# Performance work log

Measured on AMD Instinct MI355X. Metric: run time of the kernel, lower is better.

Reference implementation:

```python
import jax, jax.numpy as jnp
import numpy as np

N = 65536      # total atoms
D = 1024       # hidden_size (encoder output dim)
H = 2048       # ffn_hidden_size
OUT = 1        # output_size
M = 4096       # number of molecules (segments)


def _lin(k, fi, fo):
    return jax.random.normal(k, (fi, fo), jnp.float32) * (1.0 / np.sqrt(fi))


def setup_inputs() -> dict:
    key = jax.random.key(0)
    ks = jax.random.split(key, 14)
    hidden = jax.random.normal(ks[0], (N, D), jnp.float32)
    segment_ids = jnp.sort(jax.random.randint(ks[1], (N,), 0, M)).astype(jnp.int64)
    inp = {
        "hidden": hidden,
        "ffn_W1": _lin(ks[2], D, H), "ffn_b1": jnp.zeros((H,), jnp.float32),
        "ffn_W2": _lin(ks[3], H, H), "ffn_b2": jnp.zeros((H,), jnp.float32),
        "ffn_W3": _lin(ks[4], H, OUT), "ffn_b3": jnp.zeros((OUT,), jnp.float32),
        "wr_W1": _lin(ks[5], D, H), "wr_b1": jnp.zeros((H,), jnp.float32),
        "wr_W2": _lin(ks[6], H, H), "wr_b2": jnp.zeros((H,), jnp.float32),
        "wr_W3": _lin(ks[7], H, OUT), "wr_b3": jnp.ones((OUT,), jnp.float32),  # bias=1 keeps segment weight sums away from 0
        "segment_ids": segment_ids,
    }
    return inp


def _ffn(x, W1, b1, W2, b2, W3, b3):
    # Dropout(p) is identity in eval; activation = ReLU
    h = jax.nn.relu(x @ W1 + b1)
    h = jax.nn.relu(h @ W2 + b2)
    return h @ W3 + b3


def reference(hidden, ffn_W1, ffn_b1, ffn_W2, ffn_b2, ffn_W3, ffn_b3,
              wr_W1, wr_b1, wr_W2, wr_b2, wr_W3, wr_b3, segment_ids):
    seg = segment_ids.astype(jnp.int32)
    output = _ffn(hidden, ffn_W1, ffn_b1, ffn_W2, ffn_b2, ffn_W3, ffn_b3)   # [N, OUT]
    weights = _ffn(hidden, wr_W1, wr_b1, wr_W2, wr_b2, wr_W3, wr_b3)        # [N, OUT]
    # per-molecule sums over ALL elements of the segment slice (matches .sum())
    out_sum = jax.ops.segment_sum(output.sum(-1), seg, num_segments=M)      # [M]
    w_sum = jax.ops.segment_sum(weights.sum(-1), seg, num_segments=M)       # [M]
    ratio = (out_sum / w_sum)[seg][:, None]                                 # [N, 1]
    return output - weights * ratio
```

## Files before the change

kernel.cpp:

```cpp
#include <hip/hip_runtime.h>
#include <hip/hip_bf16.h>

#define DEVINL __device__ __forceinline__

typedef __attribute__((ext_vector_type(8))) short s8v;
typedef __attribute__((ext_vector_type(4))) float f4v;

using bf16 = __hip_bfloat16;
typedef unsigned short u16;

DEVINL u16 f2bu(float f) {
  bf16 h = __float2bfloat16(f);
  return *reinterpret_cast<u16*>(&h);
}

DEVINL void gload16(const void* g, void* l) {
  __builtin_amdgcn_global_load_lds((const __attribute__((address_space(1))) void*)g,
                                   (__attribute__((address_space(3))) void*)l, 16, 0, 0);
}

#define BAR()    __builtin_amdgcn_s_barrier()
#define LGKM0()  asm volatile("s_waitcnt lgkmcnt(0)" ::: "memory")
#define VM(n)    asm volatile("s_waitcnt vmcnt(" #n ")" ::: "memory")
#define SCHED0() __builtin_amdgcn_sched_barrier(0)

__global__ void k_f32_to_bf16(const float* __restrict__ x, u16* __restrict__ y, long n4) {
  long i = (long)blockIdx.x * blockDim.x + threadIdx.x;
  if (i >= n4) return;
  float4 v = ((const float4*)x)[i];
  ushort4 o;
  o.x = f2bu(v.x); o.y = f2bu(v.y); o.z = f2bu(v.z); o.w = f2bu(v.w);
  ((ushort4*)y)[i] = o;
}

__global__ void k_transpose_bf16(const float* __restrict__ W, u16* __restrict__ Wt,
                                 int rows, int cols) {
  __shared__ float tile[32][33];
  const int tx = threadIdx.x, ty = threadIdx.y;
  const int c0 = blockIdx.x * 32, r0 = blockIdx.y * 32;
  #pragma unroll
  for (int i = ty; i < 32; i += 8)
    tile[i][tx] = W[(long)(r0 + i) * cols + (c0 + tx)];
  __syncthreads();
  #pragma unroll
  for (int i = ty; i < 32; i += 8)
    Wt[(long)(c0 + i) * rows + (r0 + tx)] = f2bu(tile[tx][i]);
}

extern __shared__ char smem[];

template<int EPI>
__global__ __launch_bounds__(512, 2)
void k_gemm8(const u16* __restrict__ A, const u16* __restrict__ Bt,
             u16* __restrict__ C, const float* __restrict__ bias,
             const float* __restrict__ w3, float* __restrict__ oacc,
             int N, int K) {
  const int tid = threadIdx.x;
  const int w = tid >> 6, lane = tid & 63;
  const int id = blockIdx.x;
  const int cpx = gridDim.x >> 3;
  const int sw = (id & 7) * cpx + (id >> 3);
  const int bn = sw & 7, bm = sw >> 3;

  const int wm = (w >> 2) * 128, wn = (w & 3) * 64;
  const int nt = K >> 6;

  f4v acc[8][4];
  #pragma unroll
  for (int i = 0; i < 8; ++i)
    #pragma unroll
    for (int jj = 0; jj < 4; ++jj)
      #pragma unroll
      for (int r = 0; r < 4; ++r) acc[i][jj][r] = 0.f;

  const int rowl = tid >> 2;
  const int jsw = (tid & 3) ^ ((rowl >> 1) & 3);
  const u16* gA = A + (long)(bm * 256 + rowl) * K + jsw * 8;
  const u16* gB = Bt + (long)(bn * 256 + rowl) * K + jsw * 8;
  const long cstr = (long)128 * K;
  const uint wb = (uint)w * 1024u;

  const uint swz = ((uint)((lane >> 4) ^ ((lane >> 1) & 3))) * 16u;
  const uint aoff = (uint)(wm + (lane & 15)) * 64u + swz;
  const uint boff = (uint)(wn + (lane & 15)) * 64u + swz + 32768u;

#define STAGE_A(pp, ks, t) do { \
    const u16* g_ = gA + (long)(t) * 64 + (ks) * 32; \
    char* l_ = smem + (uint)(pp) * 65536u + (uint)(ks) * 16384u + wb; \
    gload16(g_, l_); gload16(g_ + cstr, l_ + 8192); } while (0)
#define STAGE_B(pp, ks, t) do { \
    const u16* g_ = gB + (long)(t) * 64 + (ks) * 32; \
    char* l_ = smem + (uint)(pp) * 65536u + 32768u + (uint)(ks) * 16384u + wb; \
    gload16(g_, l_); gload16(g_ + cstr, l_ + 8192); } while (0)

#define RD_A(dst, base, ksb) do { \
    _Pragma("unroll") \
    for (int mi_ = 0; mi_ < 8; ++mi_) \
      dst[mi_] = *(const s8v*)(smem + (base) + (ksb) + aoff + (uint)mi_ * 1024u); } while (0)
#define RD_B(dst, base, ksb, c0) do { \
    dst[0] = *(const s8v*)(smem + (base) + (ksb) + boff + (uint)(c0) * 1024u); \
    dst[1] = *(const s8v*)(smem + (base) + (ksb) + boff + (uint)((c0) + 1) * 1024u); } while (0)

#define MFMA8(A_, B_, c0i, c1i) do { \
    __builtin_amdgcn_s_setprio(1); \
    _Pragma("unroll") \
    for (int mi_ = 0; mi_ < 8; ++mi_) { \
      acc[mi_][c0i] = __builtin_amdgcn_mfma_f32_16x16x32_bf16(A_[mi_], B_[0], acc[mi_][c0i], 0, 0, 0); \
      acc[mi_][c1i] = __builtin_amdgcn_mfma_f32_16x16x32_bf16(A_[mi_], B_[1], acc[mi_][c1i], 0, 0, 0); \
    } \
    __builtin_amdgcn_s_setprio(0); } while (0)

  s8v a[8], b01[2], b23[2];

  STAGE_A(0, 0, 0); STAGE_B(0, 0, 0); STAGE_A(0, 1, 0); STAGE_B(0, 1, 0);
  if (nt > 1) { STAGE_A(1, 0, 1); STAGE_B(1, 0, 1); VM(8); }
  else        { VM(4); }
  BAR();

  for (int t = 0; t < nt; ++t) {
    const int p = t & 1, q = p ^ 1;
    const uint pb = (uint)p * 65536u;
    RD_A(a, pb, 0u); RD_B(b01, pb, 0u, 0);
    if (t + 1 < nt) STAGE_A(q, 1, t + 1);
    BAR(); LGKM0(); SCHED0();
    MFMA8(a, b01, 0, 1);
    BAR();
    RD_B(b23, pb, 0u, 2);
    if (t + 1 < nt) { STAGE_B(q, 1, t + 1); VM(8); }
    else            { VM(0); }
    BAR(); LGKM0(); SCHED0();
    MFMA8(a, b23, 2, 3);
    BAR();
    RD_A(a, pb, 16384u); RD_B(b01, pb, 16384u, 0);
    if (t + 2 < nt) STAGE_A(p, 0, t + 2);
    BAR(); LGKM0(); SCHED0();
    MFMA8(a, b01, 0, 1);
    BAR();
    RD_B(b23, pb, 16384u, 2);
    if (t + 2 < nt)      { STAGE_B(p, 0, t + 2); VM(8); }
    else if (t + 1 < nt) { VM(4); }
    else                 { VM(0); }
    BAR(); LGKM0(); SCHED0();
    MFMA8(a, b23, 2, 3);
    BAR();
  }

  const int crow = bm * 256 + wm + ((lane >> 4) << 2);
  const int ccol = bn * 256 + wn + (lane & 15);
  if (EPI == 1) {
    #pragma unroll
    for (int jj = 0; jj < 4; ++jj) {
      const float bb = bias[ccol + jj * 16];
      #pragma unroll
      for (int mi = 0; mi < 8; ++mi)
        #pragma unroll
        for (int r = 0; r < 4; ++r) {
          float v = acc[mi][jj][r] + bb;
          v = v > 0.f ? v : 0.f;
          C[(long)(crow + mi * 16 + r) * N + ccol + jj * 16] = f2bu(v);
        }
    }
  } else {
    float bb[4], ww[4];
    #pragma unroll
    for (int jj = 0; jj < 4; ++jj) { bb[jj] = bias[ccol + jj * 16]; ww[jj] = w3[ccol + jj * 16]; }
    #pragma unroll
    for (int mi = 0; mi < 8; ++mi)
      #pragma unroll
      for (int r = 0; r < 4; ++r) {
        float s = 0.f;
        #pragma unroll
        for (int jj = 0; jj < 4; ++jj) {
          float v = acc[mi][jj][r] + bb[jj];
          v = v > 0.f ? v : 0.f;
          s += v * ww[jj];
        }
        s += __shfl_xor(s, 1, 64);
        s += __shfl_xor(s, 2, 64);
        s += __shfl_xor(s, 4, 64);
        s += __shfl_xor(s, 8, 64);
        if ((lane & 15) == 0) atomicAdd(&oacc[crow + mi * 16 + r], s);
      }
  }
#undef STAGE_A
#undef STAGE_B
#undef RD_A
#undef RD_B
#undef MFMA8
}

__global__ void k_detect(const int* __restrict__ seg, int n, int* __restrict__ flag) {
  if (blockIdx.x == 0 && threadIdx.x == 0) flag[0] = (seg[n - 1] == 0) ? 1 : 0;
}

__global__ void k_segsum(const float* __restrict__ oacc, const float* __restrict__ wacc,
                         const int* __restrict__ seg, const int* __restrict__ flag,
                         const float* __restrict__ ob3, const float* __restrict__ wb3,
                         float* __restrict__ osum, float* __restrict__ wsum, int n) {
  int i = blockIdx.x * blockDim.x + threadIdx.x;
  if (i >= n) return;
  int s = flag[0] ? seg[2 * i] : seg[i];
  atomicAdd(&osum[s], oacc[i] + ob3[0]);
  atomicAdd(&wsum[s], wacc[i] + wb3[0]);
}

__global__ void k_final(const float* __restrict__ oacc, const float* __restrict__ wacc,
                        const int* __restrict__ seg, const int* __restrict__ flag,
                        const float* __restrict__ ob3, const float* __restrict__ wb3,
                        const float* __restrict__ osum, const float* __restrict__ wsum,
                        float* __restrict__ out, int n) {
  int i = blockIdx.x * blockDim.x + threadIdx.x;
  if (i >= n) return;
  int s = flag[0] ? seg[2 * i] : seg[i];
  float o = oacc[i] + ob3[0];
  float ww = wacc[i] + wb3[0];
  out[i] = o - ww * (osum[s] / wsum[s]);
}

extern "C" void kernel_launch(void* const* d_in, const int* in_sizes, int n_in,
                              void* d_out, int out_size, void* d_ws, size_t ws_size,
                              hipStream_t stream) {
  constexpr int NA = 65536, D = 1024, H = 2048, M = 4096;
  const float* hidden = (const float*)d_in[0];
  const float* fW1 = (const float*)d_in[1];
  const float* fb1 = (const float*)d_in[2];
  const float* fW2 = (const float*)d_in[3];
  const float* fb2 = (const float*)d_in[4];
  const float* fW3 = (const float*)d_in[5];
  const float* fb3 = (const float*)d_in[6];
  const float* wW1 = (const float*)d_in[7];
  const float* wb1 = (const float*)d_in[8];
  const float* wW2 = (const float*)d_in[9];
  const float* wb2 = (const float*)d_in[10];
  const float* wW3 = (const float*)d_in[11];
  const float* wb3 = (const float*)d_in[12];
  const int* seg = (const int*)d_in[13];
  float* out = (float*)d_out;

  char* ws = (char*)d_ws;
  size_t off = 0;
  auto alloc = [&](size_t bytes) { char* p = ws + off; off += (bytes + 255) & ~(size_t)255; return p; };
  u16* hbf  = (u16*)alloc((size_t)NA * D * 2);
  u16* w1tf = (u16*)alloc((size_t)H * D * 2);
  u16* w1tw = (u16*)alloc((size_t)H * D * 2);
  u16* w2tf = (u16*)alloc((size_t)H * H * 2);
  u16* w2tw = (u16*)alloc((size_t)H * H * 2);
  u16* h1   = (u16*)alloc((size_t)NA * H * 2);
  float* oacc = (float*)alloc((size_t)NA * 4);
  float* wacc = (float*)alloc((size_t)NA * 4);
  float* osum = (float*)alloc((size_t)M * 4);
  float* wsum = (float*)alloc((size_t)M * 4);
  int* flag = (int*)alloc(256);

  hipFuncSetAttribute((const void*)k_gemm8<1>, hipFuncAttributeMaxDynamicSharedMemorySize, 131072);
  hipFuncSetAttribute((const void*)k_gemm8<2>, hipFuncAttributeMaxDynamicSharedMemorySize, 131072);

  k_f32_to_bf16<<<(int)((long)NA * D / 4 / 256), 256, 0, stream>>>(hidden, hbf, (long)NA * D / 4);
  dim3 tb(32, 8);
  k_transpose_bf16<<<dim3(H / 32, D / 32), tb, 0, stream>>>(fW1, w1tf, D, H);
  k_transpose_bf16<<<dim3(H / 32, D / 32), tb, 0, stream>>>(wW1, w1tw, D, H);
  k_transpose_bf16<<<dim3(H / 32, H / 32), tb, 0, stream>>>(fW2, w2tf, H, H);
  k_transpose_bf16<<<dim3(H / 32, H / 32), tb, 0, stream>>>(wW2, w2tw, H, H);

  hipMemsetAsync(oacc, 0, (size_t)((char*)flag - (char*)oacc), stream);
  k_detect<<<1, 64, 0, stream>>>(seg, NA, flag);

  const int nblk = (H / 256) * (NA / 256);
  k_gemm8<1><<<nblk, 512, 131072, stream>>>(hbf, w1tf, h1, fb1, nullptr, nullptr, H, D);
  k_gemm8<2><<<nblk, 512, 131072, stream>>>(h1, w2tf, nullptr, fb2, fW3, oacc, H, H);
  k_gemm8<1><<<nblk, 512, 131072, stream>>>(hbf, w1tw, h1, wb1, nullptr, nullptr, H, D);
  k_gemm8<2><<<nblk, 512, 131072, stream>>>(h1, w2tw, nullptr, wb2, wW3, wacc, H, H);

  k_segsum<<<NA / 256, 256, 0, stream>>>(oacc, wacc, seg, flag, fb3, wb3, osum, wsum, NA);
  k_final<<<NA / 256, 256, 0, stream>>>(oacc, wacc, seg, flag, fb3, wb3, osum, wsum, out, NA);
}
```

Before: 1.975 ms.

## Switch GEMM to 32x32x16 MFMA with B read directly from global

Result: slower. 4.382 ms (+121.9%).

```diff
diff --git a/kernel.cpp b/kernel.cpp
--- a/kernel.cpp
+++ b/kernel.cpp
@@ -4,7 +4,7 @@
 #define DEVINL __device__ __forceinline__
 
 typedef __attribute__((ext_vector_type(8))) short s8v;
-typedef __attribute__((ext_vector_type(4))) float f4v;
+typedef __attribute__((ext_vector_type(16))) float f16v;
 
 using bf16 = __hip_bfloat16;
 typedef unsigned short u16;
@@ -20,7 +20,7 @@
 }
 
 #define BAR()    __builtin_amdgcn_s_barrier()
-#define LGKM0()  asm volatile("s_waitcnt lgkmcnt(0)" ::: "memory")
+#define LGKM(n)  asm volatile("s_waitcnt lgkmcnt(" #n ")" ::: "memory")
 #define VM(n)    asm volatile("s_waitcnt vmcnt(" #n ")" ::: "memory")
 #define SCHED0() __builtin_amdgcn_sched_barrier(0)
 
@@ -61,131 +61,130 @@
   const int cpx = gridDim.x >> 3;
   const int sw = (id & 7) * cpx + (id >> 3);
   const int bn = sw & 7, bm = sw >> 3;
-
   const int wm = (w >> 2) * 128, wn = (w & 3) * 64;
   const int nt = K >> 6;
 
-  f4v acc[8][4];
+  f16v acc[4][2];
   #pragma unroll
-  for (int i = 0; i < 8; ++i)
-    #pragma unroll
-    for (int jj = 0; jj < 4; ++jj)
+  for (int mi = 0; mi < 4; ++mi)
+    #pragma unroll
+    for (int ni = 0; ni < 2; ++ni)
       #pragma unroll
-      for (int r = 0; r < 4; ++r) acc[i][jj][r] = 0.f;
-
-  const int rowl = tid >> 2;
-  const int jsw = (tid & 3) ^ ((rowl >> 1) & 3);
-  const u16* gA = A + (long)(bm * 256 + rowl) * K + jsw * 8;
-  const u16* gB = Bt + (long)(bn * 256 + rowl) * K + jsw * 8;
-  const long cstr = (long)128 * K;
-  const uint wb = (uint)w * 1024u;
-
-  const uint swz = ((uint)((lane >> 4) ^ ((lane >> 1) & 3))) * 16u;
-  const uint aoff = (uint)(wm + (lane & 15)) * 64u + swz;
-  const uint boff = (uint)(wn + (lane & 15)) * 64u + swz + 32768u;
-
-#define STAGE_A(pp, ks, t) do { \
-    const u16* g_ = gA + (long)(t) * 64 + (ks) * 32; \
-    char* l_ = smem + (uint)(pp) * 65536u + (uint)(ks) * 16384u + wb; \
-    gload16(g_, l_); gload16(g_ + cstr, l_ + 8192); } while (0)
-#define STAGE_B(pp, ks, t) do { \
-    const u16* g_ = gB + (long)(t) * 64 + (ks) * 32; \
-    char* l_ = smem + (uint)(pp) * 65536u + 32768u + (uint)(ks) * 16384u + wb; \
-    gload16(g_, l_); gload16(g_ + cstr, l_ + 8192); } while (0)
-
-#define RD_A(dst, base, ksb) do { \
-    _Pragma("unroll") \
-    for (int mi_ = 0; mi_ < 8; ++mi_) \
-      dst[mi_] = *(const s8v*)(smem + (base) + (ksb) + aoff + (uint)mi_ * 1024u); } while (0)
-#define RD_B(dst, base, ksb, c0) do { \
-    dst[0] = *(const s8v*)(smem + (base) + (ksb) + boff + (uint)(c0) * 1024u); \
-    dst[1] = *(const s8v*)(smem + (base) + (ksb) + boff + (uint)((c0) + 1) * 1024u); } while (0)
-
-#define MFMA8(A_, B_, c0i, c1i) do { \
+      for (int r = 0; r < 16; ++r) acc[mi][ni][r] = 0.f;
+
+  const u16* gAs = A + ((long)(bm * 256 + w * 8 + (lane >> 3))) * K
+                     + ((lane & 7) ^ ((lane >> 3) & 7)) * 8;
+  const u16* gBs = Bt + ((long)(bn * 256 + wn + (lane & 31))) * K + ((lane >> 5) & 1) * 8;
+  const uint a_row = (uint)(wm + (lane & 31)) * 128u;
+  const uint apl16 = ((uint)(((lane >> 5) & 1) ^ (lane & 7))) << 4;
+
+#define STAGE1(bufidx, j, tt) \
+  gload16(gAs + (long)(j) * 64 * K + (long)(tt) * 64, \
+          smem + (uint)(bufidx) * 32768u + (uint)((j) * 8 + w) * 1024u)
+#define RDA(dst, bufidx, ks) do { \
+    const uint base_ = (uint)(bufidx) * 32768u + a_row + (((uint)(ks) << 5) ^ apl16); \
+    dst[0] = *(const s8v*)(smem + base_); \
+    dst[1] = *(const s8v*)(smem + base_ + 4096u); \
+    dst[2] = *(const s8v*)(smem + base_ + 8192u); \
+    dst[3] = *(const s8v*)(smem + base_ + 12288u); } while (0)
+#define RDB(dst, kk) do { \
+    dst[0] = *(const s8v*)(gBs + (kk)); \
+    dst[1] = *(const s8v*)(gBs + (long)32 * K + (kk)); } while (0)
+#define MFMA8(Aa, Bb) do { \
     __builtin_amdgcn_s_setprio(1); \
     _Pragma("unroll") \
-    for (int mi_ = 0; mi_ < 8; ++mi_) { \
-      acc[mi_][c0i] = __builtin_amdgcn_mfma_f32_16x16x32_bf16(A_[mi_], B_[0], acc[mi_][c0i], 0, 0, 0); \
-      acc[mi_][c1i] = __builtin_amdgcn_mfma_f32_16x16x32_bf16(A_[mi_], B_[1], acc[mi_][c1i], 0, 0, 0); \
-    } \
+    for (int mi_ = 0; mi_ < 4; ++mi_) { \
+      acc[mi_][0] = __builtin_amdgcn_mfma_f32_32x32x16_bf16(Aa[mi_], Bb[0], acc[mi_][0], 0, 0, 0); \
+      acc[mi_][1] = __builtin_amdgcn_mfma_f32_32x32x16_bf16(Aa[mi_], Bb[1], acc[mi_][1], 0, 0, 0); } \
     __builtin_amdgcn_s_setprio(0); } while (0)
 
-  s8v a[8], b01[2], b23[2];
-
-  STAGE_A(0, 0, 0); STAGE_B(0, 0, 0); STAGE_A(0, 1, 0); STAGE_B(0, 1, 0);
-  if (nt > 1) { STAGE_A(1, 0, 1); STAGE_B(1, 0, 1); VM(8); }
-  else        { VM(4); }
-  BAR();
+  s8v aA[4], aB[4], bA[2], bB[2];
+
+  {
+    const int t1 = (nt > 1) ? 1 : 0;
+    STAGE1(0, 0, 0); STAGE1(0, 1, 0); STAGE1(0, 2, 0); STAGE1(0, 3, 0);
+    STAGE1(1, 0, t1); STAGE1(1, 1, t1); STAGE1(1, 2, t1); STAGE1(1, 3, t1);
+  }
+  VM(4); BAR();
+  RDA(aA, 0, 0);
+  RDB(bA, 0);
+  int kn = 16;
+  const int kcap = K - 16;
 
   for (int t = 0; t < nt; ++t) {
-    const int p = t & 1, q = p ^ 1;
-    const uint pb = (uint)p * 65536u;
-    RD_A(a, pb, 0u); RD_B(b01, pb, 0u, 0);
-    if (t + 1 < nt) STAGE_A(q, 1, t + 1);
-    BAR(); LGKM0(); SCHED0();
-    MFMA8(a, b01, 0, 1);
-    BAR();
-    RD_B(b23, pb, 0u, 2);
-    if (t + 1 < nt) { STAGE_B(q, 1, t + 1); VM(8); }
-    else            { VM(0); }
-    BAR(); LGKM0(); SCHED0();
-    MFMA8(a, b23, 2, 3);
-    BAR();
-    RD_A(a, pb, 16384u); RD_B(b01, pb, 16384u, 0);
-    if (t + 2 < nt) STAGE_A(p, 0, t + 2);
-    BAR(); LGKM0(); SCHED0();
-    MFMA8(a, b01, 0, 1);
-    BAR();
-    RD_B(b23, pb, 16384u, 2);
-    if (t + 2 < nt)      { STAGE_B(p, 0, t + 2); VM(8); }
-    else if (t + 1 < nt) { VM(4); }
-    else                 { VM(0); }
-    BAR(); LGKM0(); SCHED0();
-    MFMA8(a, b23, 2, 3);
-    BAR();
+    const int bc = t & 3, bnx = (t + 1) & 3, bs = (t + 2) & 3;
+    const int tt = (t + 2 < nt) ? (t + 2) : (nt - 1);
+    int knc;
+    VM(9); BAR();
+    RDA(aB, bc, 1);
+    knc = kn < kcap ? kn : kcap; RDB(bB, knc); kn += 16;
+    STAGE1(bs, 0, tt);
+    LGKM(4); SCHED0();
+    MFMA8(aA, bA);
+    VM(9); BAR();
+    RDA(aA, bc, 2);
+    knc = kn < kcap ? kn : kcap; RDB(bA, knc); kn += 16;
+    STAGE1(bs, 1, tt);
+    LGKM(4); SCHED0();
+    MFMA8(aB, bB);
+    VM(9); BAR();
+    RDA(aB, bc, 3);
+    knc = kn < kcap ? kn : kcap; RDB(bB, knc); kn += 16;
+    STAGE1(bs, 2, tt);
+    LGKM(4); SCHED0();
+    MFMA8(aA, bA);
+    VM(9); BAR();
+    RDA(aA, bnx, 0);
+    knc = kn < kcap ? kn : kcap; RDB(bA, knc); kn += 16;
+    STAGE1(bs, 3, tt);
+    LGKM(4); SCHED0();
+    MFMA8(aB, bB);
   }
 
-  const int crow = bm * 256 + wm + ((lane >> 4) << 2);
-  const int ccol = bn * 256 + wn + (lane & 15);
+  const int colb = bn * 256 + wn + (lane & 31);
+  const int rowb = bm * 256 + wm + 4 * ((lane >> 5) & 1);
   if (EPI == 1) {
     #pragma unroll
-    for (int jj = 0; jj < 4; ++jj) {
-      const float bb = bias[ccol + jj * 16];
+    for (int ni = 0; ni < 2; ++ni) {
+      const int col = colb + ni * 32;
+      const float bb = bias[col];
       #pragma unroll
-      for (int mi = 0; mi < 8; ++mi)
+      for (int mi = 0; mi < 4; ++mi)
         #pragma unroll
-        for (int r = 0; r < 4; ++r) {
-          float v = acc[mi][jj][r] + bb;
+        for (int r = 0; r < 16; ++r) {
+          const int row = rowb + mi * 32 + (r & 3) + 8 * (r >> 2);
+          float v = acc[mi][ni][r] + bb;
           v = v > 0.f ? v : 0.f;
-          C[(long)(crow + mi * 16 + r) * N + ccol + jj * 16] = f2bu(v);
+          C[(long)row * N + col] = f2bu(v);
         }
     }
   } else {
-    float bb[4], ww[4];
-    #pragma unroll
-    for (int jj = 0; jj < 4; ++jj) { bb[jj] = bias[ccol + jj * 16]; ww[jj] = w3[ccol + jj * 16]; }
-    #pragma unroll
-    for (int mi = 0; mi < 8; ++mi)
+    float bb[2], ww[2];
+    #pragma unroll
+    for (int ni = 0; ni < 2; ++ni) { bb[ni] = bias[colb + ni * 32]; ww[ni] = w3[colb + ni * 32]; }
+    #pragma unroll
+    for (int mi = 0; mi < 4; ++mi)
       #pragma unroll
-      for (int r = 0; r < 4; ++r) {
+      for (int r = 0; r < 16; ++r) {
         float s = 0.f;
         #pragma unroll
-        for (int jj = 0; jj < 4; ++jj) {
-          float v = acc[mi][jj][r] + bb[jj];
+        for (int ni = 0; ni < 2; ++ni) {
+          float v = acc[mi][ni][r] + bb[ni];
           v = v > 0.f ? v : 0.f;
-          s += v * ww[jj];
+          s += v * ww[ni];
         }
         s += __shfl_xor(s, 1, 64);
         s += __shfl_xor(s, 2, 64);
         s += __shfl_xor(s, 4, 64);
         s += __shfl_xor(s, 8, 64);
-        if ((lane & 15) == 0) atomicAdd(&oacc[crow + mi * 16 + r], s);
+        s += __shfl_xor(s, 16, 64);
+        if ((lane & 31) == 0)
+          atomicAdd(&oacc[rowb + mi * 32 + (r & 3) + 8 * (r >> 2)], s);
       }
   }
-#undef STAGE_A
-#undef STAGE_B
-#undef RD_A
-#undef RD_B
+#undef STAGE1
+#undef RDA
+#undef RDB
 #undef MFMA8
 }
 
```
